# Performance work log

Measured on AMD Instinct MI355X. Metric: run time of the kernel, lower is better.

The kernel has to match this reference:

```python
import jax, jax.numpy as jnp
import numpy as np

EPS = 1e-5

def _layer_norm(x, gamma, beta):
    mu = jnp.mean(x, axis=-1, keepdims=True)
    var = jnp.var(x, axis=-1, keepdims=True)
    return (x - mu) * jax.lax.rsqrt(var + EPS) * gamma + beta

def setup_inputs() -> dict:
    key = jax.random.key(0)
    ks = jax.random.split(key, 4)
    B, T, D, H = 16, 2048, 1024, 1024
    s_in = 1.0 / np.sqrt(D)
    return {
        "x": jax.random.normal(ks[0], (B, T, D), dtype=jnp.float32),
        "c": jnp.zeros((B, H), dtype=jnp.float32),
        "W_lt": jax.random.uniform(ks[1], (H, D), jnp.float32, -s_in, s_in),
        "W_g": jax.random.uniform(ks[2], (2 * H, D), jnp.float32, -s_in, s_in),
        "b_g": jnp.zeros((2 * H,), dtype=jnp.float32),
        "gamma_g": jnp.ones((2 * H,), dtype=jnp.float32),
        "beta_g": jnp.zeros((2 * H,), dtype=jnp.float32),
        "gamma_a": jnp.ones((H,), dtype=jnp.float32),
        "beta_a": jnp.zeros((H,), dtype=jnp.float32),
    }

def reference(x, c, W_lt, W_g, b_g, gamma_g, beta_g, gamma_a, beta_a):
    H = W_lt.shape[0]
    # x: [B,T,D]
    x_tilde = jnp.einsum("btd,hd->bth", x, W_lt)            # [B,T,H]
    gate = jax.nn.sigmoid(_layer_norm(jnp.einsum("btd,gd->btg", x, W_g) + b_g, gamma_g, beta_g))
    f = gate[:, :, :H]                                        # forget gate [B,T,H]
    r = gate[:, :, H:]                                        # reset gate  [B,T,H]
    new_data = (1.0 - f) * x_tilde

    def step(c_prev, ft_nd):
        f_t, nd_t = ft_nd
        c_t = f_t * c_prev + nd_t
        return c_t, c_t

    # scan over time: move T to leading axis
    c_final, all_c = jax.lax.scan(step, c, (jnp.swapaxes(f, 0, 1), jnp.swapaxes(new_data, 0, 1)))
    all_c = jnp.swapaxes(all_c, 0, 1)                         # [B,T,H]
    h = r * jax.nn.sigmoid(_layer_norm(all_c, gamma_a, beta_a)) + (1.0 - r) * x
    return (h, c_final)
```

## Files before the change

### kernel.cpp

```cpp
#include <hip/hip_runtime.h>
#include <stdint.h>

typedef unsigned short u16;
typedef u16 us8 __attribute__((ext_vector_type(8)));
typedef uint32_t u32x8 __attribute__((ext_vector_type(8)));
typedef __bf16 bf16x8 __attribute__((ext_vector_type(8)));
typedef float f32x4 __attribute__((ext_vector_type(4)));

#define BB 16
#define TT 2048
#define HH 1024
#define MM 32768
#define NN 3072
#define KK 1024
#define NT 16

__device__ __forceinline__ float b2f(u16 u) {
    union { uint32_t i; float f; } v; v.i = ((uint32_t)u) << 16; return v.f;
}
__device__ __forceinline__ u16 f2b(float f) {
    union { uint32_t i; float f; } v; v.f = f;
    uint32_t r = v.i + 0x7fffu + ((v.i >> 16) & 1u);
    return (u16)(r >> 16);
}
__device__ __forceinline__ float sigm(float z) {
    return 1.f / (1.f + __expf(-z));
}
__device__ __forceinline__ void load_lds16(const u16* g, u16* l) {
    __builtin_amdgcn_global_load_lds(
        (const __attribute__((address_space(1))) void*)g,
        (__attribute__((address_space(3))) void*)l, 16, 0, 0);
}
__device__ __forceinline__ f32x4 mf(bf16x8 a, bf16x8 b, f32x4 c) {
    return __builtin_amdgcn_mfma_f32_16x16x32_bf16(a, b, c, 0, 0, 0);
}

__global__ __launch_bounds__(256) void k_cvt(const float* __restrict__ x,
                                             const float* __restrict__ wlt,
                                             const float* __restrict__ wg,
                                             u16* __restrict__ xb,
                                             u16* __restrict__ wb) {
    long i = (long)(blockIdx.x * 256 + threadIdx.x) * 8;
    const float* s;
    u16* o;
    if (i < 33554432L) { s = x + i; o = xb + i; }
    else {
        long j = i - 33554432L;
        s = (j < 1048576L) ? (wlt + j) : (wg + (j - 1048576L));
        o = wb + j;
    }
    float4 a = *(const float4*)(s);
    float4 b = *(const float4*)(s + 4);
    us8 r;
    r[0] = f2b(a.x); r[1] = f2b(a.y); r[2] = f2b(a.z); r[3] = f2b(a.w);
    r[4] = f2b(b.x); r[5] = f2b(b.y); r[6] = f2b(b.z); r[7] = f2b(b.w);
    *(us8*)o = r;
}

__global__ __launch_bounds__(512, 2) void k_gemm(const u16* __restrict__ A,
                                                 const u16* __restrict__ W,
                                                 u16* __restrict__ Y) {
    __shared__ u16 As[2 * 16384];
    __shared__ u16 Bs[2 * 16384];
    const int tid = threadIdx.x;
    const int lane = tid & 63;
    const int w = tid >> 6;
    const int wm = w >> 2;
    const int wn = w & 3;
    const int q = lane >> 4;
    const int l16 = lane & 15;
    const int bx = blockIdx.x;
    const int by = blockIdx.y;

    const int slog = ((tid & 7) ^ ((tid >> 3) & 7)) << 3;
    const u16* aS = A + (size_t)(by * 256 + (tid >> 3)) * KK + slog;
    const u16* bS = W + (size_t)(bx * 256 + ((tid >> 8) << 6) + ((tid >> 3) & 31)) * KK + slog;
    u16* aD = As + w * 512;
    u16* bD = Bs + w * 512;

    load_lds16(aS,                aD);
    load_lds16(aS + 128 * KK,     aD + 4096);
    load_lds16(aS + 64 * KK,      aD + 8192);
    load_lds16(aS + 192 * KK,     aD + 12288);
    load_lds16(bS,                bD);
    load_lds16(bS + 128 * KK,     bD + 4096);
    load_lds16(bS + 32 * KK,      bD + 8192);
    load_lds16(bS + 160 * KK,     bD + 12288);
    load_lds16(aS + 64,           aD + 16384);
    load_lds16(aS + 64 + 128*KK,  aD + 16384 + 4096);
    load_lds16(aS + 64 + 64*KK,   aD + 16384 + 8192);
    load_lds16(aS + 64 + 192*KK,  aD + 16384 + 12288);
    load_lds16(bS + 64,           bD + 16384);
    load_lds16(bS + 64 + 128*KK,  bD + 16384 + 4096);
    load_lds16(bS + 64 + 32*KK,   bD + 16384 + 8192);
    load_lds16(bS + 64 + 160*KK,  bD + 16384 + 12288);

    const int key = l16 & 7;
    const int sA0 = ((q ^ key) << 3);
    const int sA1 = (((q ^ key) ^ 4) << 3);
    const int aB0 = wm * 4096 + l16 * 64 + sA0;
    const int aB1 = wm * 4096 + l16 * 64 + sA1;
    const int bB0 = wn * 2048 + l16 * 64 + sA0;
    const int bB1 = wn * 2048 + l16 * 64 + sA1;

    f32x4 zero = {0.f, 0.f, 0.f, 0.f};
    f32x4 acc[8][4];
#pragma unroll
    for (int i = 0; i < 8; ++i)
#pragma unroll
        for (int j = 0; j < 4; ++j) acc[i][j] = zero;
    bf16x8 aR[4][2], bR[4][2];

    asm volatile("s_waitcnt vmcnt(8)" ::: "memory");
    __builtin_amdgcn_sched_barrier(0);
    __builtin_amdgcn_s_barrier();
    asm volatile("" ::: "memory");

    for (int kt = 0; kt < NT; ++kt) {
        const int cb = (kt & 1) << 14;
        const int kc = (kt + 2) << 6;
#pragma unroll
        for (int i = 0; i < 4; ++i) {
            aR[i][0] = *(const bf16x8*)&As[cb + i * 1024 + aB0];
            aR[i][1] = *(const bf16x8*)&As[cb + i * 1024 + aB1];
        }
#pragma unroll
        for (int f = 0; f < 4; ++f) {
            bR[f][0] = *(const bf16x8*)&Bs[cb + (f >> 1) * 8192 + (f & 1) * 1024 + bB0];
            bR[f][1] = *(const bf16x8*)&Bs[cb + (f >> 1) * 8192 + (f & 1) * 1024 + bB1];
        }
        asm volatile("" ::: "memory");
        __builtin_amdgcn_s_barrier();
        asm volatile("s_waitcnt lgkmcnt(0)" ::: "memory");
        __builtin_amdgcn_sched_barrier(0);
        __builtin_amdgcn_s_setprio(1);
#pragma unroll
        for (int i = 0; i < 4; ++i)
#pragma unroll
            for (int f = 0; f < 2; ++f) {
                acc[i][f] = mf(aR[i][0], bR[f][0], acc[i][f]);
                acc[i][f] = mf(aR[i][1], bR[f][1], acc[i][f]);
            }
        __builtin_amdgcn_s_setprio(0);
        asm volatile("" ::: "memory");
        __builtin_amdgcn_s_barrier();
        asm volatile("" ::: "memory");
        if (kt < NT - 2) {
            load_lds16(aS + kc,            aD + cb);
            load_lds16(aS + kc + 128*KK,   aD + cb + 4096);
            load_lds16(bS + kc,            bD + cb);
            load_lds16(bS + kc + 128*KK,   bD + cb + 4096);
            load_lds16(bS + kc + 32*KK,    bD + cb + 8192);
            load_lds16(bS + kc + 160*KK,   bD + cb + 12288);
        }
        asm volatile("" ::: "memory");
        __builtin_amdgcn_s_barrier();
        __builtin_amdgcn_s_setprio(1);
#pragma unroll
        for (int i = 0; i < 4; ++i)
#pragma unroll
            for (int f = 2; f < 4; ++f) {
                acc[i][f] = mf(aR[i][0], bR[f][0], acc[i][f]);
                acc[i][f] = mf(aR[i][1], bR[f][1], acc[i][f]);
            }
        __builtin_amdgcn_s_setprio(0);
        asm volatile("" ::: "memory");
        __builtin_amdgcn_s_barrier();
        asm volatile("" ::: "memory");
#pragma unroll
        for (int i = 0; i < 4; ++i) {
            aR[i][0] = *(const bf16x8*)&As[cb + 8192 + i * 1024 + aB0];
            aR[i][1] = *(const bf16x8*)&As[cb + 8192 + i * 1024 + aB1];
        }
        asm volatile("" ::: "memory");
        __builtin_amdgcn_s_barrier();
        asm volatile("s_waitcnt lgkmcnt(0)" ::: "memory");
        __builtin_amdgcn_sched_barrier(0);
        __builtin_amdgcn_s_setprio(1);
#pragma unroll
        for (int i = 0; i < 4; ++i)
#pragma unroll
            for (int f = 0; f < 2; ++f) {
                acc[4 + i][f] = mf(aR[i][0], bR[f][0], acc[4 + i][f]);
                acc[4 + i][f] = mf(aR[i][1], bR[f][1], acc[4 + i][f]);
            }
        __builtin_amdgcn_s_setprio(0);
        asm volatile("" ::: "memory");
        __builtin_amdgcn_s_barrier();
        asm volatile("" ::: "memory");
        if (kt < NT - 2) {
            load_lds16(aS + kc + 64*KK,    aD + cb + 8192);
            load_lds16(aS + kc + 192*KK,   aD + cb + 12288);
        }
        asm volatile("" ::: "memory");
        __builtin_amdgcn_s_barrier();
        __builtin_amdgcn_s_setprio(1);
#pragma unroll
        for (int i = 0; i < 4; ++i)
#pragma unroll
            for (int f = 2; f < 4; ++f) {
                acc[4 + i][f] = mf(aR[i][0], bR[f][0], acc[4 + i][f]);
                acc[4 + i][f] = mf(aR[i][1], bR[f][1], acc[4 + i][f]);
            }
        __builtin_amdgcn_s_setprio(0);
        if (kt < NT - 2) { asm volatile("s_waitcnt vmcnt(8)" ::: "memory"); }
        else             { asm volatile("s_waitcnt vmcnt(0)" ::: "memory"); }
        __builtin_amdgcn_sched_barrier(0);
        __builtin_amdgcn_s_barrier();
        asm volatile("" ::: "memory");
    }

#pragma unroll
    for (int fm = 0; fm < 8; ++fm) {
#pragma unroll
        for (int rg = 0; rg < 4; ++rg) {
            const int row = by * 256 + wm * 128 + fm * 16 + q * 4 + rg;
            u16* yp = Y + (size_t)row * NN + bx * 256 + wn * 64 + l16;
#pragma unroll
            for (int fn = 0; fn < 4; ++fn) yp[fn * 16] = f2b(acc[fm][fn][rg]);
        }
    }
}

__global__ __launch_bounds__(256) void k_lnsig(const u16* __restrict__ Y,
                                               const float* __restrict__ bg,
                                               const float* __restrict__ gg,
                                               const float* __restrict__ bt,
                                               uint32_t* __restrict__ FN,
                                               u16* __restrict__ R) {
    const int row = blockIdx.x;
    const int t = threadIdx.x;
    const u16* yr = Y + (size_t)row * 3072;
    us8 gv = *(const us8*)(yr + 1024 + t * 8);
    float z[8];
    float s = 0.f, s2 = 0.f;
#pragma unroll
    for (int k = 0; k < 8; k++) {
        z[k] = b2f(gv[k]) + bg[t * 8 + k];
        s += z[k];
        s2 += z[k] * z[k];
    }
#pragma unroll
    for (int m = 1; m < 64; m <<= 1) {
        s += __shfl_xor(s, m);
        s2 += __shfl_xor(s2, m);
    }
    __shared__ float red[8];
    if ((t & 63) == 0) { red[t >> 6] = s; red[(t >> 6) + 4] = s2; }
    __syncthreads();
    s = red[0] + red[1] + red[2] + red[3];
    s2 = red[4] + red[5] + red[6] + red[7];
    const float mu = s * (1.f / 2048.f);
    const float inv = rsqrtf(s2 * (1.f / 2048.f) - mu * mu + 1e-5f);
    float gate[8];
#pragma unroll
    for (int k = 0; k < 8; k++)
        gate[k] = sigm((z[k] - mu) * inv * gg[t * 8 + k] + bt[t * 8 + k]);
    if (t < 128) {
        us8 xt = *(const us8*)(yr + t * 8);
        u32x8 fn;
#pragma unroll
        for (int k = 0; k < 8; k++) {
            u16 fb = f2b(gate[k]);
            u16 nb = f2b((1.f - gate[k]) * b2f(xt[k]));
            fn[k] = (uint32_t)fb | ((uint32_t)nb << 16);
        }
        *(u32x8*)(FN + (size_t)row * 1024 + t * 8) = fn;
    } else {
        us8 ro;
#pragma unroll
        for (int k = 0; k < 8; k++) ro[k] = f2b(gate[k]);
        *(us8*)(R + (size_t)row * 1024 + (t - 128) * 8) = ro;
    }
}

__global__ __launch_bounds__(256) void k_scan1(const uint32_t* __restrict__ FN,
                                               float2* __restrict__ agg) {
    int u = blockIdx.x * 256 + threadIdx.x;
    int h2 = u & 511;
    int chunk = (u >> 9) & 31;
    int b = u >> 14;
    size_t base = (size_t)(b * 2048 + chunk * 64) * 1024 + h2 * 2;
    float F0 = 1.f, N0 = 0.f, F1 = 1.f, N1 = 0.f;
#pragma unroll 4
    for (int i = 0; i < 64; i++) {
        uint2 v = *(const uint2*)(FN + base + (size_t)i * 1024);
        float f0 = b2f((u16)(v.x & 0xffffu)), n0 = b2f((u16)(v.x >> 16));
        float f1 = b2f((u16)(v.y & 0xffffu)), n1 = b2f((u16)(v.y >> 16));
        N0 = fmaf(f0, N0, n0); F0 *= f0;
        N1 = fmaf(f1, N1, n1); F1 *= f1;
    }
    float4 o = {F0, N0, F1, N1};
    *(float4*)&agg[(size_t)(b * 32 + chunk) * 1024 + h2 * 2] = o;
}

__global__ __launch_bounds__(256) void k_scan2(const float2* __restrict__ agg,
                                               const float* __restrict__ c0,
                                               float* __restrict__ P) {
    int u = blockIdx.x * 256 + threadIdx.x;
    int b = u >> 10, h = u & 1023;
    float c = c0[u];
#pragma unroll 4
    for (int k = 0; k < 32; k++) {
        size_t idx = (size_t)(b * 32 + k) * 1024 + h;
        P[idx] = c;
        float2 fn = agg[idx];
        c = fmaf(fn.x, c, fn.y);
    }
}

__global__ __launch_bounds__(512) void k_scanout(const uint32_t* __restrict__ FN,
                                                 const float* __restrict__ P,
                                                 const u16* __restrict__ R,
                                                 const u16* __restrict__ xb,
                                                 const float* __restrict__ ga,
                                                 const float* __restrict__ ba,
                                                 float* __restrict__ out,
                                                 float* __restrict__ cfin) {
    __shared__ float2 red[2][8];
    const int t = threadIdx.x;
    const int b = blockIdx.x >> 5, chunk = blockIdx.x & 31;
    const int h = t * 2;
    const int w = t >> 6, lane = t & 63;
    float2 cp = *(const float2*)&P[(size_t)(b * 32 + chunk) * 1024 + h];
    float c0 = cp.x, c1 = cp.y;
    const float g0 = ga[h], g1 = ga[h + 1];
    const float be0 = ba[h], be1 = ba[h + 1];
    const size_t base = (size_t)(b * 2048 + chunk * 64) * 1024 + h;
#pragma unroll 2
    for (int i = 0; i < 64; i++) {
        const size_t ro = base + (size_t)i * 1024;
        uint2 fn = *(const uint2*)(FN + ro);
        uint32_t rv = *(const uint32_t*)(R + ro);
        uint32_t xv = *(const uint32_t*)(xb + ro);
        c0 = fmaf(b2f((u16)(fn.x & 0xffffu)), c0, b2f((u16)(fn.x >> 16)));
        c1 = fmaf(b2f((u16)(fn.y & 0xffffu)), c1, b2f((u16)(fn.y >> 16)));
        float s = c0 + c1, s2 = c0 * c0 + c1 * c1;
#pragma unroll
        for (int m = 1; m < 64; m <<= 1) {
            s += __shfl_xor(s, m);
            s2 += __shfl_xor(s2, m);
        }
        const int p = i & 1;
        if (lane == 0) red[p][w] = make_float2(s, s2);
        __syncthreads();
        s = 0.f; s2 = 0.f;
#pragma unroll
        for (int k = 0; k < 8; k++) { float2 v = red[p][k]; s += v.x; s2 += v.y; }
        const float mu = s * (1.f / 1024.f);
        const float inv = rsqrtf(s2 * (1.f / 1024.f) - mu * mu + 1e-5f);
        const float sg0 = sigm((c0 - mu) * inv * g0 + be0);
        const float sg1 = sigm((c1 - mu) * inv * g1 + be1);
        const float r0 = b2f((u16)(rv & 0xffffu)), r1 = b2f((u16)(rv >> 16));
        const float x0 = b2f((u16)(xv & 0xffffu)), x1 = b2f((u16)(xv >> 16));
        float2 ho = {r0 * sg0 + (1.f - r0) * x0, r1 * sg1 + (1.f - r1) * x1};
        *(float2*)(out + ro) = ho;
    }
    if (chunk == 31) *(float2*)(cfin + b * 1024 + h) = make_float2(c0, c1);
}

extern "C" void kernel_launch(void* const* d_in, const int* in_sizes, int n_in,
                              void* d_out, int out_size, void* d_ws, size_t ws_size,
                              hipStream_t stream) {
    const float* x   = (const float*)d_in[0];
    const float* c0  = (const float*)d_in[1];
    const float* wlt = (const float*)d_in[2];
    const float* wg  = (const float*)d_in[3];
    const float* bg  = (const float*)d_in[4];
    const float* gg  = (const float*)d_in[5];
    const float* btg = (const float*)d_in[6];
    const float* ga  = (const float*)d_in[7];
    const float* ba  = (const float*)d_in[8];
    float* out = (float*)d_out;

    char* ws = (char*)d_ws;
    u16* xb      = (u16*)(ws);
    u16* wb      = (u16*)(ws + 67108864);
    u16* y       = (u16*)(ws + 73400320);
    uint32_t* FN = (uint32_t*)(ws + 274726912);
    u16* R       = (u16*)(ws + 408944640);
    float2* agg  = (float2*)(ws + 476053504);
    float* P     = (float*)(ws + 480247808);

    k_cvt<<<17920, 256, 0, stream>>>(x, wlt, wg, xb, wb);
    k_gemm<<<dim3(NN / 256, MM / 256), 512, 0, stream>>>(xb, wb, y);
    k_lnsig<<<32768, 256, 0, stream>>>(y, bg, gg, btg, FN, R);
    k_scan1<<<1024, 256, 0, stream>>>(FN, agg);
    k_scan2<<<64, 256, 0, stream>>>(agg, c0, P);
    k_scanout<<<512, 512, 0, stream>>>(FN, P, R, xb, ga, ba, out,
                                       out + (size_t)33554432);
}
```

Baseline: 669.1 us.

## Retune GEMM pipeline, swizzle block order, prefetch in scan-output kernel

The GEMM remaps block indices with an XCD-style swizzle so neighbouring tiles share L2. It splits B-fragment LDS reads into lo/hi halves interleaved with the MFMA phases and peels the last k-iteration. The scan-output kernel software-prefetches the next two rows' loads and swaps __syncthreads for a raw s_barrier. The gate kernel hoists its x_tilde load and two scan loops get larger unroll factors. Together these aim to hide LDS and global latency, at the cost of more registers and fragile hand-placed waitcnt ordering.

```diff
diff --git a/kernel.cpp b/kernel.cpp
--- a/kernel.cpp
+++ b/kernel.cpp
@@ -34,6 +34,7 @@
 __device__ __forceinline__ f32x4 mf(bf16x8 a, bf16x8 b, f32x4 c) {
     return __builtin_amdgcn_mfma_f32_16x16x32_bf16(a, b, c, 0, 0, 0);
 }
+#define MEMBAR() asm volatile("" ::: "memory")
 
 __global__ __launch_bounds__(256) void k_cvt(const float* __restrict__ x,
                                              const float* __restrict__ wlt,
@@ -69,8 +70,11 @@
     const int wn = w & 3;
     const int q = lane >> 4;
     const int l16 = lane & 15;
-    const int bx = blockIdx.x;
-    const int by = blockIdx.y;
+
+    const unsigned bid = blockIdx.y * 12u + blockIdx.x;
+    const unsigned sw = (bid & 7u) * 192u + (bid >> 3);
+    const int by = sw / 12u;
+    const int bx = sw % 12u;
 
     const int slog = ((tid & 7) ^ ((tid >> 3) & 7)) << 3;
     const u16* aS = A + (size_t)(by * 256 + (tid >> 3)) * KK + slog;
@@ -109,105 +113,158 @@
     for (int i = 0; i < 8; ++i)
 #pragma unroll
         for (int j = 0; j < 4; ++j) acc[i][j] = zero;
-    bf16x8 aR[4][2], bR[4][2];
+    bf16x8 aX[4], aY[4], bLo[4], bHi[4];
 
     asm volatile("s_waitcnt vmcnt(8)" ::: "memory");
     __builtin_amdgcn_sched_barrier(0);
     __builtin_amdgcn_s_barrier();
-    asm volatile("" ::: "memory");
-
-    for (int kt = 0; kt < NT; ++kt) {
+    MEMBAR();
+
+    for (int kt = 0; kt < NT - 1; ++kt) {
         const int cb = (kt & 1) << 14;
         const int kc = (kt + 2) << 6;
-#pragma unroll
-        for (int i = 0; i < 4; ++i) {
-            aR[i][0] = *(const bf16x8*)&As[cb + i * 1024 + aB0];
-            aR[i][1] = *(const bf16x8*)&As[cb + i * 1024 + aB1];
-        }
-#pragma unroll
-        for (int f = 0; f < 4; ++f) {
-            bR[f][0] = *(const bf16x8*)&Bs[cb + (f >> 1) * 8192 + (f & 1) * 1024 + bB0];
-            bR[f][1] = *(const bf16x8*)&Bs[cb + (f >> 1) * 8192 + (f & 1) * 1024 + bB1];
-        }
-        asm volatile("" ::: "memory");
+        const bool st = (kt < NT - 2);
+#pragma unroll
+        for (int i = 0; i < 4; ++i) {
+            aX[i] = *(const bf16x8*)&As[cb + i * 1024 + aB0];
+            aY[i] = *(const bf16x8*)&As[cb + i * 1024 + aB1];
+        }
+        bLo[0] = *(const bf16x8*)&Bs[cb + bB0];
+        bLo[1] = *(const bf16x8*)&Bs[cb + bB1];
+        bLo[2] = *(const bf16x8*)&Bs[cb + 1024 + bB0];
+        bLo[3] = *(const bf16x8*)&Bs[cb + 1024 + bB1];
+        asm volatile("s_waitcnt lgkmcnt(8)" ::: "memory");
+        __builtin_amdgcn_sched_barrier(0);
         __builtin_amdgcn_s_barrier();
         asm volatile("s_waitcnt lgkmcnt(0)" ::: "memory");
         __builtin_amdgcn_sched_barrier(0);
         __builtin_amdgcn_s_setprio(1);
 #pragma unroll
-        for (int i = 0; i < 4; ++i)
-#pragma unroll
-            for (int f = 0; f < 2; ++f) {
-                acc[i][f] = mf(aR[i][0], bR[f][0], acc[i][f]);
-                acc[i][f] = mf(aR[i][1], bR[f][1], acc[i][f]);
-            }
+        for (int i = 0; i < 4; ++i) {
+            acc[i][0] = mf(aX[i], bLo[0], acc[i][0]);
+            acc[i][0] = mf(aY[i], bLo[1], acc[i][0]);
+            acc[i][1] = mf(aX[i], bLo[2], acc[i][1]);
+            acc[i][1] = mf(aY[i], bLo[3], acc[i][1]);
+        }
         __builtin_amdgcn_s_setprio(0);
-        asm volatile("" ::: "memory");
-        __builtin_amdgcn_s_barrier();
-        asm volatile("" ::: "memory");
-        if (kt < NT - 2) {
+        MEMBAR();
+        __builtin_amdgcn_s_barrier();
+        MEMBAR();
+        bHi[0] = *(const bf16x8*)&Bs[cb + 8192 + bB0];
+        bHi[1] = *(const bf16x8*)&Bs[cb + 8192 + bB1];
+        bHi[2] = *(const bf16x8*)&Bs[cb + 8192 + 1024 + bB0];
+        bHi[3] = *(const bf16x8*)&Bs[cb + 8192 + 1024 + bB1];
+        if (st) {
             load_lds16(aS + kc,            aD + cb);
             load_lds16(aS + kc + 128*KK,   aD + cb + 4096);
             load_lds16(bS + kc,            bD + cb);
             load_lds16(bS + kc + 128*KK,   bD + cb + 4096);
+        }
+        __builtin_amdgcn_sched_barrier(0);
+        __builtin_amdgcn_s_barrier();
+        asm volatile("s_waitcnt lgkmcnt(0)" ::: "memory");
+        __builtin_amdgcn_sched_barrier(0);
+        __builtin_amdgcn_s_setprio(1);
+#pragma unroll
+        for (int i = 0; i < 4; ++i) {
+            acc[i][2] = mf(aX[i], bHi[0], acc[i][2]);
+            acc[i][2] = mf(aY[i], bHi[1], acc[i][2]);
+            acc[i][3] = mf(aX[i], bHi[2], acc[i][3]);
+            acc[i][3] = mf(aY[i], bHi[3], acc[i][3]);
+        }
+        __builtin_amdgcn_s_setprio(0);
+        MEMBAR();
+        __builtin_amdgcn_s_barrier();
+        MEMBAR();
+#pragma unroll
+        for (int i = 0; i < 4; ++i) {
+            aX[i] = *(const bf16x8*)&As[cb + 8192 + i * 1024 + aB0];
+            aY[i] = *(const bf16x8*)&As[cb + 8192 + i * 1024 + aB1];
+        }
+        if (st) {
             load_lds16(bS + kc + 32*KK,    bD + cb + 8192);
             load_lds16(bS + kc + 160*KK,   bD + cb + 12288);
         }
-        asm volatile("" ::: "memory");
-        __builtin_amdgcn_s_barrier();
+        __builtin_amdgcn_sched_barrier(0);
+        __builtin_amdgcn_s_barrier();
+        asm volatile("s_waitcnt lgkmcnt(0)" ::: "memory");
+        __builtin_amdgcn_sched_barrier(0);
         __builtin_amdgcn_s_setprio(1);
 #pragma unroll
-        for (int i = 0; i < 4; ++i)
-#pragma unroll
-            for (int f = 2; f < 4; ++f) {
-                acc[i][f] = mf(aR[i][0], bR[f][0], acc[i][f]);
-                acc[i][f] = mf(aR[i][1], bR[f][1], acc[i][f]);
-            }
+        for (int i = 0; i < 4; ++i) {
+            acc[4 + i][0] = mf(aX[i], bLo[0], acc[4 + i][0]);
+            acc[4 + i][0] = mf(aY[i], bLo[1], acc[4 + i][0]);
+            acc[4 + i][1] = mf(aX[i], bLo[2], acc[4 + i][1]);
+            acc[4 + i][1] = mf(aY[i], bLo[3], acc[4 + i][1]);
+        }
         __builtin_amdgcn_s_setprio(0);
-        asm volatile("" ::: "memory");
-        __builtin_amdgcn_s_barrier();
-        asm volatile("" ::: "memory");
-#pragma unroll
-        for (int i = 0; i < 4; ++i) {
-            aR[i][0] = *(const bf16x8*)&As[cb + 8192 + i * 1024 + aB0];
-            aR[i][1] = *(const bf16x8*)&As[cb + 8192 + i * 1024 + aB1];
-        }
-        asm volatile("" ::: "memory");
-        __builtin_amdgcn_s_barrier();
-        asm volatile("s_waitcnt lgkmcnt(0)" ::: "memory");
-        __builtin_amdgcn_sched_barrier(0);
-        __builtin_amdgcn_s_setprio(1);
-#pragma unroll
-        for (int i = 0; i < 4; ++i)
-#pragma unroll
-            for (int f = 0; f < 2; ++f) {
-                acc[4 + i][f] = mf(aR[i][0], bR[f][0], acc[4 + i][f]);
-                acc[4 + i][f] = mf(aR[i][1], bR[f][1], acc[4 + i][f]);
-            }
-        __builtin_amdgcn_s_setprio(0);
-        asm volatile("" ::: "memory");
-        __builtin_amdgcn_s_barrier();
-        asm volatile("" ::: "memory");
-        if (kt < NT - 2) {
+        MEMBAR();
+        __builtin_amdgcn_s_barrier();
+        MEMBAR();
+        if (st) {
             load_lds16(aS + kc + 64*KK,    aD + cb + 8192);
             load_lds16(aS + kc + 192*KK,   aD + cb + 12288);
         }
-        asm volatile("" ::: "memory");
+        __builtin_amdgcn_sched_barrier(0);
         __builtin_amdgcn_s_barrier();
         __builtin_amdgcn_s_setprio(1);
 #pragma unroll
-        for (int i = 0; i < 4; ++i)
-#pragma unroll
-            for (int f = 2; f < 4; ++f) {
-                acc[4 + i][f] = mf(aR[i][0], bR[f][0], acc[4 + i][f]);
-                acc[4 + i][f] = mf(aR[i][1], bR[f][1], acc[4 + i][f]);
-            }
+        for (int i = 0; i < 4; ++i) {
+            acc[4 + i][2] = mf(aX[i], bHi[0], acc[4 + i][2]);
+            acc[4 + i][2] = mf(aY[i], bHi[1], acc[4 + i][2]);
+            acc[4 + i][3] = mf(aX[i], bHi[2], acc[4 + i][3]);
+            acc[4 + i][3] = mf(aY[i], bHi[3], acc[4 + i][3]);
+        }
         __builtin_amdgcn_s_setprio(0);
-        if (kt < NT - 2) { asm volatile("s_waitcnt vmcnt(8)" ::: "memory"); }
-        else             { asm volatile("s_waitcnt vmcnt(0)" ::: "memory"); }
-        __builtin_amdgcn_sched_barrier(0);
-        __builtin_amdgcn_s_barrier();
-        asm volatile("" ::: "memory");
+        if (st) { asm volatile("s_waitcnt vmcnt(8)" ::: "memory"); }
+        else    { asm volatile("s_waitcnt vmcnt(0)" ::: "memory"); }
+        __builtin_amdgcn_sched_barrier(0);
+        __builtin_amdgcn_s_barrier();
+        MEMBAR();
+    }
+
+    {
+        const int cb = 16384;
+#pragma unroll
+        for (int i = 0; i < 4; ++i) {
+            aX[i] = *(const bf16x8*)&As[cb + i * 1024 + aB0];
+            aY[i] = *(const bf16x8*)&As[cb + i * 1024 + aB1];
+        }
+        bLo[0] = *(const bf16x8*)&Bs[cb + bB0];
+        bLo[1] = *(const bf16x8*)&Bs[cb + bB1];
+        bLo[2] = *(const bf16x8*)&Bs[cb + 1024 + bB0];
+        bLo[3] = *(const bf16x8*)&Bs[cb + 1024 + bB1];
+        bHi[0] = *(const bf16x8*)&Bs[cb + 8192 + bB0];
+        bHi[1] = *(const bf16x8*)&Bs[cb + 8192 + bB1];
+        bHi[2] = *(const bf16x8*)&Bs[cb + 8192 + 1024 + bB0];
+        bHi[3] = *(const bf16x8*)&Bs[cb + 8192 + 1024 + bB1];
+#pragma unroll
+        for (int i = 0; i < 4; ++i) {
+            acc[i][0] = mf(aX[i], bLo[0], acc[i][0]);
+            acc[i][0] = mf(aY[i], bLo[1], acc[i][0]);
+            acc[i][1] = mf(aX[i], bLo[2], acc[i][1]);
+            acc[i][1] = mf(aY[i], bLo[3], acc[i][1]);
+            acc[i][2] = mf(aX[i], bHi[0], acc[i][2]);
+            acc[i][2] = mf(aY[i], bHi[1], acc[i][2]);
+            acc[i][3] = mf(aX[i], bHi[2], acc[i][3]);
+            acc[i][3] = mf(aY[i], bHi[3], acc[i][3]);
+        }
+#pragma unroll
+        for (int i = 0; i < 4; ++i) {
+            aX[i] = *(const bf16x8*)&As[cb + 8192 + i * 1024 + aB0];
+            aY[i] = *(const bf16x8*)&As[cb + 8192 + i * 1024 + aB1];
+        }
+#pragma unroll
+        for (int i = 0; i < 4; ++i) {
+            acc[4 + i][0] = mf(aX[i], bLo[0], acc[4 + i][0]);
+            acc[4 + i][0] = mf(aY[i], bLo[1], acc[4 + i][0]);
+            acc[4 + i][1] = mf(aX[i], bLo[2], acc[4 + i][1]);
+            acc[4 + i][1] = mf(aY[i], bLo[3], acc[4 + i][1]);
+            acc[4 + i][2] = mf(aX[i], bHi[0], acc[4 + i][2]);
+            acc[4 + i][2] = mf(aY[i], bHi[1], acc[4 + i][2]);
+            acc[4 + i][3] = mf(aX[i], bHi[2], acc[4 + i][3]);
+            acc[4 + i][3] = mf(aY[i], bHi[3], acc[4 + i][3]);
+        }
     }
 
 #pragma unroll
@@ -232,6 +289,8 @@
     const int t = threadIdx.x;
     const u16* yr = Y + (size_t)row * 3072;
     us8 gv = *(const us8*)(yr + 1024 + t * 8);
+    us8 xt;
+    if (t < 128) xt = *(const us8*)(yr + t * 8);
     float z[8];
     float s = 0.f, s2 = 0.f;
 #pragma unroll
@@ -247,7 +306,10 @@
     }
     __shared__ float red[8];
     if ((t & 63) == 0) { red[t >> 6] = s; red[(t >> 6) + 4] = s2; }
-    __syncthreads();
+    asm volatile("s_waitcnt lgkmcnt(0)" ::: "memory");
+    __builtin_amdgcn_sched_barrier(0);
+    __builtin_amdgcn_s_barrier();
+    MEMBAR();
     s = red[0] + red[1] + red[2] + red[3];
     s2 = red[4] + red[5] + red[6] + red[7];
     const float mu = s * (1.f / 2048.f);
@@ -257,7 +319,6 @@
     for (int k = 0; k < 8; k++)
         gate[k] = sigm((z[k] - mu) * inv * gg[t * 8 + k] + bt[t * 8 + k]);
     if (t < 128) {
-        us8 xt = *(const us8*)(yr + t * 8);
         u32x8 fn;
 #pragma unroll
         for (int k = 0; k < 8; k++) {
@@ -282,7 +343,7 @@
     int b = u >> 14;
     size_t base = (size_t)(b * 2048 + chunk * 64) * 1024 + h2 * 2;
     float F0 = 1.f, N0 = 0.f, F1 = 1.f, N1 = 0.f;
-#pragma unroll 4
+#pragma unroll 8
     for (int i = 0; i < 64; i++) {
         uint2 v = *(const uint2*)(FN + base + (size_t)i * 1024);
         float f0 = b2f((u16)(v.x & 0xffffu)), n0 = b2f((u16)(v.x >> 16));
@@ -300,7 +361,7 @@
     int u = blockIdx.x * 256 + threadIdx.x;
     int b = u >> 10, h = u & 1023;
     float c = c0[u];
-#pragma unroll 4
+#pragma unroll 8
     for (int k = 0; k < 32; k++) {
         size_t idx = (size_t)(b * 32 + k) * 1024 + h;
         P[idx] = c;
@@ -308,6 +369,34 @@
         c = fmaf(fn.x, c, fn.y);
     }
 }
+
+#define SOUT_STEP(fnv, rvv, xvv, ro, p)                                        \
+    {                                                                          \
+        c0 = fmaf(b2f((u16)((fnv).x & 0xffffu)), c0, b2f((u16)((fnv).x >> 16)));\
+        c1 = fmaf(b2f((u16)((fnv).y & 0xffffu)), c1, b2f((u16)((fnv).y >> 16)));\
+        float s = c0 + c1, s2 = c0 * c0 + c1 * c1;                             \
+        _Pragma("unroll")                                                      \
+        for (int m = 1; m < 64; m <<= 1) {                                     \
+            s += __shfl_xor(s, m);                                             \
+            s2 += __shfl_xor(s2, m);                                           \
+        }                                                                      \
+        if (lane == 0) red[p][w] = make_float2(s, s2);                         \
+        asm volatile("s_waitcnt lgkmcnt(0)" ::: "memory");                     \
+        __builtin_amdgcn_sched_barrier(0);                                     \
+        __builtin_amdgcn_s_barrier();                                          \
+        MEMBAR();                                                              \
+        s = 0.f; s2 = 0.f;                                                     \
+        _Pragma("unroll")                                                      \
+        for (int k = 0; k < 8; k++) { float2 v = red[p][k]; s += v.x; s2 += v.y; } \
+        const float mu = s * (1.f / 1024.f);                                   \
+        const float inv = rsqrtf(s2 * (1.f / 1024.f) - mu * mu + 1e-5f);       \
+        const float sg0 = sigm((c0 - mu) * inv * g0 + be0);                    \
+        const float sg1 = sigm((c1 - mu) * inv * g1 + be1);                    \
+        const float r0 = b2f((u16)((rvv) & 0xffffu)), r1 = b2f((u16)((rvv) >> 16)); \
+        const float x0 = b2f((u16)((xvv) & 0xffffu)), x1 = b2f((u16)((xvv) >> 16)); \
+        float2 ho = {r0 * sg0 + (1.f - r0) * x0, r1 * sg1 + (1.f - r1) * x1};  \
+        *(float2*)(out + (ro)) = ho;                                           \
+    }
 
 __global__ __launch_bounds__(512) void k_scanout(const uint32_t* __restrict__ FN,
                                                  const float* __restrict__ P,
@@ -327,34 +416,36 @@
     const float g0 = ga[h], g1 = ga[h + 1];
     const float be0 = ba[h], be1 = ba[h + 1];
     const size_t base = (size_t)(b * 2048 + chunk * 64) * 1024 + h;
-#pragma unroll 2
-    for (int i = 0; i < 64; i++) {
-        const size_t ro = base + (size_t)i * 1024;
-        uint2 fn = *(const uint2*)(FN + ro);
-        uint32_t rv = *(const uint32_t*)(R + ro);
-        uint32_t xv = *(const uint32_t*)(xb + ro);
-        c0 = fmaf(b2f((u16)(fn.x & 0xffffu)), c0, b2f((u16)(fn.x >> 16)));
-        c1 = fmaf(b2f((u16)(fn.y & 0xffffu)), c1, b2f((u16)(fn.y >> 16)));
-        float s = c0 + c1, s2 = c0 * c0 + c1 * c1;
-#pragma unroll
-        for (int m = 1; m < 64; m <<= 1) {
-            s += __shfl_xor(s, m);
-            s2 += __shfl_xor(s2, m);
-        }
-        const int p = i & 1;
-        if (lane == 0) red[p][w] = make_float2(s, s2);
-        __syncthreads();
-        s = 0.f; s2 = 0.f;
-#pragma unroll
-        for (int k = 0; k < 8; k++) { float2 v = red[p][k]; s += v.x; s2 += v.y; }
-        const float mu = s * (1.f / 1024.f);
-        const float inv = rsqrtf(s2 * (1.f / 1024.f) - mu * mu + 1e-5f);
-        const float sg0 = sigm((c0 - mu) * inv * g0 + be0);
-        const float sg1 = sigm((c1 - mu) * inv * g1 + be1);
-        const float r0 = b2f((u16)(rv & 0xffffu)), r1 = b2f((u16)(rv >> 16));
-        const float x0 = b2f((u16)(xv & 0xffffu)), x1 = b2f((u16)(xv >> 16));
-        float2 ho = {r0 * sg0 + (1.f - r0) * x0, r1 * sg1 + (1.f - r1) * x1};
-        *(float2*)(out + ro) = ho;
+
+    uint2 fnA = *(const uint2*)(FN + base);
+    uint32_t rvA = *(const uint32_t*)(R + base);
+    uint32_t xvA = *(const uint32_t*)(xb + base);
+    uint2 fnB = *(const uint2*)(FN + base + 1024);
+    uint32_t rvB = *(const uint32_t*)(R + base + 1024);
+    uint32_t xvB = *(const uint32_t*)(xb + base + 1024);
+
+    for (int ii = 0; ii < 32; ++ii) {
+        const size_t ro0 = base + (size_t)(2 * ii) * 1024;
+        {
+            uint2 fn = fnA; uint32_t rv = rvA, xv = xvA;
+            if (ii < 31) {
+                const size_t rn = ro0 + 2048;
+                fnA = *(const uint2*)(FN + rn);
+                rvA = *(const uint32_t*)(R + rn);
+                xvA = *(const uint32_t*)(xb + rn);
+            }
+            SOUT_STEP(fn, rv, xv, ro0, 0)
+        }
+        {
+            uint2 fn = fnB; uint32_t rv = rvB, xv = xvB;
+            if (ii < 31) {
+                const size_t rn = ro0 + 3072;
+                fnB = *(const uint2*)(FN + rn);
+                rvB = *(const uint32_t*)(R + rn);
+                xvB = *(const uint32_t*)(xb + rn);
+            }
+            SOUT_STEP(fn, rv, xv, ro0 + 1024, 1)
+        }
     }
     if (chunk == 31) *(float2*)(cfin + b * 1024 + h) = make_float2(c0, c1);
 }
```

New measurement: 632.3 us. -5.5%, faster.
